# Kernel tuning notes

Hardware: AMD Instinct MI355X
Metric: run time of the kernel (lower is better)

The kernel has to match this reference:

```python
import jax, jax.numpy as jnp
import numpy as np

H, L, D, R = 16, 4096, 64, 128   # heads, seq len, head dim, FAVOR+ feature dim
S_SCALE = 0.125                  # attention inner-product scaling S
CHUNK = 128                      # chunk size for causal linear attention
EPS = 1e-10                      # module's self.epsilon denominator guard


def _get_proj(d, r, seed=0):
    # get_proj(R, D, orthogonal=True, hyperbolic=True): QR-orthogonalized
    # Gaussian block rescaled by chi column norms, then [W, -W].
    rng = np.random.RandomState(seed)
    rh = r // 2
    w = rng.randn(d, rh)
    chis = np.linalg.norm(w, ord=2, axis=0, keepdims=True)
    qm, _ = np.linalg.qr(w, mode='reduced')
    w = qm * chis
    return np.concatenate((w, -w), axis=1).astype(np.float32)  # (D, R)


def setup_inputs() -> dict:
    key = jax.random.key(0)
    kq, kk, kv = jax.random.split(key, 3)
    q = jax.random.normal(kq, (H, L, D), dtype=jnp.float32)
    k = jax.random.normal(kk, (H, L, D), dtype=jnp.float32)
    v = jax.random.normal(kv, (H, L, D), dtype=jnp.float32)
    W = jnp.asarray(_get_proj(D, R))
    return {"T": 64, "k": k, "q": q, "v": v, "W": W}


def _phi(x, W):
    # FAVOR+ feature map: x' = x * S^0.5 / D^0.25;
    # phi(x) = exp(W^T x' - ||x'||^2 / 2) / sqrt(R)
    xs = x * (S_SCALE ** 0.5 / D ** 0.25)            # (H, L, D)
    Wx = jnp.einsum('hld,dr->hlr', xs, W)            # (H, L, R)
    sq = 0.5 * jnp.sum(xs * xs, axis=-1, keepdims=True)
    return jnp.exp(Wx - sq) / (R ** 0.5)             # (H, L, R)


def reference(T, k, q, v, W):
    # Deterministic FAVOR+ estimator of the strictly-causal softmax attention
    # Pred_l = sum_{j<l} v_j exp(S<q_l,k_j>) / sum_{i<l} exp(S<q_l,k_i>)
    # which the tree+sampling machinery approximates (T = sampling budget,
    # irrelevant for the exact kernel estimate). Chunked linear attention.
    del T
    pq = _phi(q, W)                                  # (H, L, R)
    pk = _phi(k, W)                                  # (H, L, R)
    nc = L // CHUNK
    pq_c = pq.reshape(H, nc, CHUNK, R)
    pk_c = pk.reshape(H, nc, CHUNK, R)
    v_c = v.reshape(H, nc, CHUNK, D)
    # per-chunk KV summaries and exclusive prefix over chunks
    skv = jnp.einsum('hncr,hncd->hnrd', pk_c, v_c)   # (H, nc, R, D)
    zk = jnp.sum(pk_c, axis=2)                       # (H, nc, R)
    skv_prev = jnp.cumsum(skv, axis=1) - skv         # exclusive
    zk_prev = jnp.cumsum(zk, axis=1) - zk
    num_inter = jnp.einsum('hncr,hnrd->hncd', pq_c, skv_prev)
    den_inter = jnp.einsum('hncr,hnr->hnc', pq_c, zk_prev)
    # intra-chunk strictly-causal part (j < l)
    A = jnp.einsum('hncr,hnsr->hncs', pq_c, pk_c)    # (H, nc, C, C)
    mask = jnp.tril(jnp.ones((CHUNK, CHUNK), dtype=A.dtype), k=-1)
    A = A * mask
    num_intra = jnp.einsum('hncs,hnsd->hncd', A, v_c)
    den_intra = jnp.sum(A, axis=-1)
    out = (num_inter + num_intra) / (den_inter + den_intra + EPS)[..., None]
    return out.reshape(H, L, D)
```

## Files before the change

### kernel.cpp

```cpp
#include <hip/hip_runtime.h>
#include <hip/hip_cooperative_groups.h>

namespace cg = cooperative_groups;

#define H 16
#define L 4096
#define D 64
#define R 128
#define CHUNK 128
#define NC 32
#define HL (H * L)
#define HN (H * NC)
#define EPS 1e-10f
#define XS_SCALE 0.125f
#define PHI_SCALE 0.08838834764831845f

typedef __attribute__((ext_vector_type(8))) short bf8;
typedef __attribute__((ext_vector_type(4))) short bf4;
typedef __attribute__((ext_vector_type(16))) float facc16;

__device__ __forceinline__ unsigned short f2b(float f) {
    unsigned u = __float_as_uint(f);
    return (unsigned short)((u + 0x7fffu + ((u >> 16) & 1u)) >> 16);
}
__device__ __forceinline__ float b2f(unsigned short s) {
    return __uint_as_float(((unsigned)s) << 16);
}

template<bool DUMP>
__device__ __forceinline__ void phase1(
    const float* __restrict__ q, const float* __restrict__ k,
    const float* __restrict__ v, const float* __restrict__ W,
    unsigned short* bufA, unsigned short* bufB, unsigned short* bufC,
    float* __restrict__ stage, float* __restrict__ zk,
    unsigned short* __restrict__ pqd, unsigned short* __restrict__ pkd,
    unsigned short* __restrict__ vTd, bf8* qf, int hn, int tid)
{
    unsigned short* Wt = bufC;
    unsigned short* xs = bufC + 8192;
    float* sq = (float*)bufB;
    const int lane = tid & 63, wave = tid >> 6, lo = lane & 31, hi = lane >> 5;
    const int l0 = wave * 32;
    const size_t cbase = (size_t)hn * CHUNK * D;

    for (int i = tid; i < 8192; i += 256) {
        int r = i & 127, d = i >> 7;
        Wt[(unsigned)((r * 64 + d) ^ ((r & 7) << 3))] = f2b(W[d * 128 + r]);
    }
    for (int i = tid; i < 2048; i += 256) {
        int row = i >> 4, d0 = (i & 15) * 4;
        float4 vv = *(const float4*)(q + cbase + row * 64 + d0);
        float a0 = vv.x * XS_SCALE, a1 = vv.y * XS_SCALE;
        float a2 = vv.z * XS_SCALE, a3 = vv.w * XS_SCALE;
        float ss = a0 * a0 + a1 * a1 + a2 * a2 + a3 * a3;
        ss += __shfl_xor(ss, 1); ss += __shfl_xor(ss, 2);
        ss += __shfl_xor(ss, 4); ss += __shfl_xor(ss, 8);
        if ((tid & 15) == 0) sq[row] = 0.5f * ss;
        unsigned idx = (unsigned)((row * 64 + d0) ^ ((row & 7) << 3));
        unsigned* p = (unsigned*)&xs[idx];
        p[0] = (unsigned)f2b(a0) | ((unsigned)f2b(a1) << 16);
        p[1] = (unsigned)f2b(a2) | ((unsigned)f2b(a3) << 16);
    }
    __syncthreads();

    {
        facc16 acc[4];
        #pragma unroll
        for (int t = 0; t < 4; ++t)
            #pragma unroll
            for (int e = 0; e < 16; ++e) acc[t][e] = 0.f;
        #pragma unroll
        for (int s = 0; s < 4; ++s) {
            const bf8 a = *(const bf8*)&xs[(unsigned)(((l0 + lo) * 64 + 16 * s + 8 * hi) ^ ((lo & 7) << 3))];
            #pragma unroll
            for (int t = 0; t < 4; ++t) {
                const bf8 b = *(const bf8*)&Wt[(unsigned)(((t * 32 + lo) * 64 + 16 * s + 8 * hi) ^ ((lo & 7) << 3))];
                acc[t] = __builtin_amdgcn_mfma_f32_32x32x16_bf16(a, b, acc[t], 0, 0, 0);
            }
        }
        #pragma unroll
        for (int t = 0; t < 4; ++t)
            #pragma unroll
            for (int reg = 0; reg < 16; ++reg) {
                int row = l0 + (reg & 3) + 8 * (reg >> 2) + 4 * hi;
                int col = t * 32 + lo;
                bufA[(unsigned)((row * 128 + col) ^ ((row & 7) << 3))] =
                    f2b(__expf(acc[t][reg] - sq[row]) * PHI_SCALE);
            }
    }
    __syncthreads();

    #pragma unroll
    for (int s = 0; s < 8; ++s)
        qf[s] = *(const bf8*)&bufA[(unsigned)(((l0 + lo) * 128 + 16 * s + 8 * hi) ^ ((lo & 7) << 3))];
    if constexpr (DUMP) {
        unsigned short* pg = pqd + (size_t)hn * CHUNK * R;
        for (int i = tid; i < 2048; i += 256) {
            int c = i >> 4, rb = (i & 15) * 8;
            *(bf8*)(pg + c * 128 + rb) = *(const bf8*)&bufA[(unsigned)((c * 128 + rb) ^ ((c & 7) << 3))];
        }
    }

    for (int i = tid; i < 2048; i += 256) {
        int row = i >> 4, d0 = (i & 15) * 4;
        float4 vv = *(const float4*)(k + cbase + row * 64 + d0);
        float a0 = vv.x * XS_SCALE, a1 = vv.y * XS_SCALE;
        float a2 = vv.z * XS_SCALE, a3 = vv.w * XS_SCALE;
        float ss = a0 * a0 + a1 * a1 + a2 * a2 + a3 * a3;
        ss += __shfl_xor(ss, 1); ss += __shfl_xor(ss, 2);
        ss += __shfl_xor(ss, 4); ss += __shfl_xor(ss, 8);
        if ((tid & 15) == 0) sq[row] = 0.5f * ss;
        unsigned idx = (unsigned)((row * 64 + d0) ^ ((row & 7) << 3));
        unsigned* p = (unsigned*)&xs[idx];
        p[0] = (unsigned)f2b(a0) | ((unsigned)f2b(a1) << 16);
        p[1] = (unsigned)f2b(a2) | ((unsigned)f2b(a3) << 16);
    }
    __syncthreads();

    facc16 acck[4];
    #pragma unroll
    for (int t = 0; t < 4; ++t)
        #pragma unroll
        for (int e = 0; e < 16; ++e) acck[t][e] = 0.f;
    #pragma unroll
    for (int s = 0; s < 4; ++s) {
        const bf8 a = *(const bf8*)&xs[(unsigned)(((l0 + lo) * 64 + 16 * s + 8 * hi) ^ ((lo & 7) << 3))];
        #pragma unroll
        for (int t = 0; t < 4; ++t) {
            const bf8 b = *(const bf8*)&Wt[(unsigned)(((t * 32 + lo) * 64 + 16 * s + 8 * hi) ^ ((lo & 7) << 3))];
            acck[t] = __builtin_amdgcn_mfma_f32_32x32x16_bf16(a, b, acck[t], 0, 0, 0);
        }
    }
    __syncthreads();

    #pragma unroll
    for (int t = 0; t < 4; ++t) {
        int colr = t * 32 + lo;
        #pragma unroll
        for (int g = 0; g < 4; ++g) {
            int c0 = l0 + 8 * g + 4 * hi;
            bf4 pk4;
            #pragma unroll
            for (int e = 0; e < 4; ++e) {
                unsigned short b = f2b(__expf(acck[t][4 * g + e] - sq[c0 + e]) * PHI_SCALE);
                pk4[e] = (short)b;
                bufA[(unsigned)(((c0 + e) * 128 + colr) ^ (((c0 + e) & 7) << 3))] = b;
            }
            *(bf4*)&bufC[(unsigned)((colr * 128 + c0) ^ ((colr & 7) << 3))] = pk4;
        }
    }
    __syncthreads();

    for (int i = tid; i < 8192; i += 256) {
        int d = i & 63, c = i >> 6;
        bufB[(unsigned)((d * 128 + c) ^ ((d & 7) << 3))] = f2b(v[cbase + c * 64 + d]);
    }
    if (tid < 128) {
        float s = 0.f;
        #pragma unroll
        for (int j = 0; j < 16; ++j) {
            bf8 a8 = *(const bf8*)&bufC[(unsigned)((tid * 128 + 8 * j) ^ ((tid & 7) << 3))];
            #pragma unroll
            for (int e = 0; e < 8; ++e) s += b2f((unsigned short)a8[e]);
        }
        zk[(size_t)hn * 128 + tid] = s;
    }
    if constexpr (DUMP) {
        unsigned short* pg = pkd + (size_t)hn * CHUNK * R;
        for (int i = tid; i < 2048; i += 256) {
            int c = i >> 4, rb = (i & 15) * 8;
            *(bf8*)(pg + c * 128 + rb) = *(const bf8*)&bufA[(unsigned)((c * 128 + rb) ^ ((c & 7) << 3))];
        }
    }
    __syncthreads();

    if constexpr (DUMP) {
        unsigned short* vg2 = vTd + (size_t)hn * D * CHUNK;
        for (int i = tid; i < 1024; i += 256) {
            int d = i >> 4, c0 = (i & 15) * 8;
            *(bf8*)(vg2 + d * 128 + c0) = *(const bf8*)&bufB[(unsigned)((d * 128 + c0) ^ ((d & 7) << 3))];
        }
    }
    {
        facc16 accs[2];
        #pragma unroll
        for (int t = 0; t < 2; ++t)
            #pragma unroll
            for (int e = 0; e < 16; ++e) accs[t][e] = 0.f;
        #pragma unroll
        for (int s = 0; s < 8; ++s) {
            const bf8 b = *(const bf8*)&bufC[(unsigned)(((wave * 32 + lo) * 128 + 16 * s + 8 * hi) ^ ((lo & 7) << 3))];
            #pragma unroll
            for (int db = 0; db < 2; ++db) {
                const bf8 a = *(const bf8*)&bufB[(unsigned)(((db * 32 + lo) * 128 + 16 * s + 8 * hi) ^ ((lo & 7) << 3))];
                accs[db] = __builtin_amdgcn_mfma_f32_32x32x16_bf16(a, b, accs[db], 0, 0, 0);
            }
        }
        float* sg = stage + (size_t)hn * D * R;
        #pragma unroll
        for (int db = 0; db < 2; ++db)
            #pragma unroll
            for (int reg = 0; reg < 16; ++reg) {
                int row = db * 32 + (reg & 3) + 8 * (reg >> 2) + 4 * hi;
                sg[row * 128 + wave * 32 + lo] = accs[db][reg];
            }
    }
}

__device__ __forceinline__ void phase2(const float* __restrict__ stage,
                                       unsigned short* __restrict__ skvTp,
                                       const float* __restrict__ zk,
                                       unsigned short* __restrict__ zkp,
                                       int bid, int tid)
{
    int g = bid * 256 + tid;
    int h2 = g >> 13, dr = g & 8191;
    const float* p = stage + (size_t)h2 * NC * 8192 + dr;
    unsigned short* o = skvTp + (size_t)h2 * NC * 8192 + dr;
    float run = 0.f;
    #pragma unroll
    for (int n = 0; n < NC; ++n) {
        float t = p[(size_t)n * 8192];
        o[(size_t)n * 8192] = f2b(run);
        run += t;
    }
    if (g < 2048) {
        int h3 = g >> 7, r = g & 127;
        const float* pz = zk + (size_t)h3 * NC * 128 + r;
        unsigned short* oz = zkp + (size_t)h3 * NC * 128 + r;
        float runz = 0.f;
        #pragma unroll
        for (int n = 0; n < NC; ++n) {
            float t2 = pz[n * 128];
            oz[n * 128] = f2b(runz);
            runz += t2;
        }
    }
}

__device__ __forceinline__ void phase3(
    unsigned short* bufA, unsigned short* bufB, unsigned short* bufC,
    const unsigned short* __restrict__ skvTp, const unsigned short* __restrict__ zkp,
    const bf8* qf, int hn, int tid, float* __restrict__ out)
{
    const int lane = tid & 63, wave = tid >> 6, lo = lane & 31, hi = lane >> 5;
    const int l0 = wave * 32;
    __syncthreads();

    const unsigned short* svg = skvTp + (size_t)hn * D * R;
    for (int i = tid; i < 1024; i += 256) {
        int d = i >> 4, r0 = (i & 15) * 8;
        *(bf8*)&bufC[(unsigned)((d * 128 + r0) ^ ((d & 7) << 3))] = *(const bf8*)(svg + d * 128 + r0);
    }
    bf8 zf[8], onesf;
    #pragma unroll
    for (int e = 0; e < 8; ++e) onesf[e] = (lo == 0) ? (short)0x3F80 : (short)0;
    #pragma unroll
    for (int s = 0; s < 8; ++s)
        #pragma unroll
        for (int e = 0; e < 8; ++e) zf[s][e] = 0;
    if (lo == 0) {
        #pragma unroll
        for (int s = 0; s < 8; ++s)
            zf[s] = *(const bf8*)(zkp + (size_t)hn * 128 + 16 * s + 8 * hi);
    }

    facc16 acc1[4];
    #pragma unroll
    for (int t = 0; t < 4; ++t)
        #pragma unroll
        for (int e = 0; e < 16; ++e) acc1[t][e] = 0.f;
    #pragma unroll
    for (int s = 0; s < 8; ++s)
        #pragma unroll
        for (int t = 0; t < 4; ++t) {
            const bf8 b = *(const bf8*)&bufA[(unsigned)(((t * 32 + lo) * 128 + 16 * s + 8 * hi) ^ ((lo & 7) << 3))];
            acc1[t] = __builtin_amdgcn_mfma_f32_32x32x16_bf16(qf[s], b, acc1[t], 0, 0, 0);
        }
    __syncthreads();

    #pragma unroll
    for (int t = 0; t < 4; ++t)
        #pragma unroll
        for (int reg = 0; reg < 16; ++reg) {
            int row = l0 + (reg & 3) + 8 * (reg >> 2) + 4 * hi;
            int sc = t * 32 + lo;
            bufA[(unsigned)((row * 128 + sc) ^ ((row & 7) << 3))] = f2b(sc < row ? acc1[t][reg] : 0.f);
        }
    __syncthreads();

    facc16 acc2[3];
    #pragma unroll
    for (int t = 0; t < 3; ++t)
        #pragma unroll
        for (int e = 0; e < 16; ++e) acc2[t][e] = 0.f;
    #pragma unroll
    for (int s = 0; s < 8; ++s) {
        const bf8 a = *(const bf8*)&bufA[(unsigned)(((l0 + lo) * 128 + 16 * s + 8 * hi) ^ ((lo & 7) << 3))];
        #pragma unroll
        for (int t = 0; t < 2; ++t) {
            const bf8 b = *(const bf8*)&bufB[(unsigned)(((t * 32 + lo) * 128 + 16 * s + 8 * hi) ^ ((lo & 7) << 3))];
            acc2[t] = __builtin_amdgcn_mfma_f32_32x32x16_bf16(a, b, acc2[t], 0, 0, 0);
        }
        acc2[2] = __builtin_amdgcn_mfma_f32_32x32x16_bf16(a, onesf, acc2[2], 0, 0, 0);
    }
    #pragma unroll
    for (int s = 0; s < 8; ++s) {
        #pragma unroll
        for (int t = 0; t < 2; ++t) {
            const bf8 b = *(const bf8*)&bufC[(unsigned)(((t * 32 + lo) * 128 + 16 * s + 8 * hi) ^ ((lo & 7) << 3))];
            acc2[t] = __builtin_amdgcn_mfma_f32_32x32x16_bf16(qf[s], b, acc2[t], 0, 0, 0);
        }
        acc2[2] = __builtin_amdgcn_mfma_f32_32x32x16_bf16(qf[s], zf[s], acc2[2], 0, 0, 0);
    }

    float* og = out + (size_t)hn * CHUNK * D;
    #pragma unroll
    for (int reg = 0; reg < 16; ++reg) {
        int row = l0 + (reg & 3) + 8 * (reg >> 2) + 4 * hi;
        float dv = __shfl(acc2[2][reg], lane & 32);
        float inv = 1.0f / (dv + EPS);
        og[row * 64 + lo]      = acc2[0][reg] * inv;
        og[row * 64 + 32 + lo] = acc2[1][reg] * inv;
    }
}

__global__ __launch_bounds__(256, 2) void fused_coop(
    const float* __restrict__ q, const float* __restrict__ k,
    const float* __restrict__ v, const float* __restrict__ W,
    unsigned short* __restrict__ skvTp, unsigned short* __restrict__ zkp,
    float* __restrict__ zk, float* __restrict__ out)
{
    __shared__ __align__(16) unsigned short LDSm[40960];
    unsigned short* bufA = LDSm;
    unsigned short* bufB = LDSm + 16384;
    unsigned short* bufC = LDSm + 24576;
    const int tid = threadIdx.x, hn = blockIdx.x;
    bf8 qf[8];
    phase1<false>(q, k, v, W, bufA, bufB, bufC, out, zk,
                  nullptr, nullptr, nullptr, qf, hn, tid);
    __threadfence();
    cg::this_grid().sync();
    phase2(out, skvTp, zk, zkp, hn, tid);
    __threadfence();
    cg::this_grid().sync();
    __threadfence();
    phase3(bufA, bufB, bufC, skvTp, zkp, qf, hn, tid, out);
}

__global__ __launch_bounds__(256, 2) void kA(
    const float* __restrict__ q, const float* __restrict__ k,
    const float* __restrict__ v, const float* __restrict__ W,
    float* __restrict__ stage, float* __restrict__ zk,
    unsigned short* __restrict__ pqd, unsigned short* __restrict__ pkd,
    unsigned short* __restrict__ vTd)
{
    __shared__ __align__(16) unsigned short LDSm[40960];
    bf8 qf[8];
    phase1<true>(q, k, v, W, LDSm, LDSm + 16384, LDSm + 24576, stage, zk,
                 pqd, pkd, vTd, qf, blockIdx.x, threadIdx.x);
}

__global__ __launch_bounds__(256) void kB(const float* __restrict__ stage,
                                          unsigned short* __restrict__ skvTp,
                                          const float* __restrict__ zk,
                                          unsigned short* __restrict__ zkp)
{
    phase2(stage, skvTp, zk, zkp, blockIdx.x, threadIdx.x);
}

__global__ __launch_bounds__(256, 2) void kC(
    const unsigned short* __restrict__ pq, const unsigned short* __restrict__ pk,
    const unsigned short* __restrict__ vT, const unsigned short* __restrict__ skvTp,
    const unsigned short* __restrict__ zkp, float* __restrict__ out)
{
    __shared__ __align__(16) unsigned short LDSm[32768];
    unsigned short* bufA = LDSm;
    unsigned short* bufB = LDSm + 16384;
    unsigned short* bufC = LDSm + 24576;
    const int tid = threadIdx.x, hn = blockIdx.x;
    const int lane = tid & 63, wave = tid >> 6, lo = lane & 31, hi = lane >> 5;
    const int l0 = wave * 32;

    bf8 qf[8];
    const unsigned short* pqg = pq + (size_t)hn * CHUNK * R;
    #pragma unroll
    for (int s = 0; s < 8; ++s)
        qf[s] = *(const bf8*)(pqg + (l0 + lo) * 128 + 16 * s + 8 * hi);

    const unsigned short* pkg = pk + (size_t)hn * CHUNK * R;
    for (int i = tid; i < 2048; i += 256) {
        int c = i >> 4, rb = (i & 15) * 8;
        *(bf8*)&bufA[(unsigned)((c * 128 + rb) ^ ((c & 7) << 3))] = *(const bf8*)(pkg + c * 128 + rb);
    }
    const unsigned short* vTg = vT + (size_t)hn * D * CHUNK;
    for (int i = tid; i < 1024; i += 256) {
        int d = i >> 4, c0 = (i & 15) * 8;
        *(bf8*)&bufB[(unsigned)((d * 128 + c0) ^ ((d & 7) << 3))] = *(const bf8*)(vTg + d * 128 + c0);
    }
    phase3(bufA, bufB, bufC, skvTp, zkp, qf, hn, tid, out);
}

extern "C" void kernel_launch(void* const* d_in, const int* in_sizes, int n_in,
                              void* d_out, int out_size, void* d_ws, size_t ws_size,
                              hipStream_t stream) {
    const float* k = (const float*)d_in[1];
    const float* q = (const float*)d_in[2];
    const float* v = (const float*)d_in[3];
    const float* W = (const float*)d_in[4];
    float* out = (float*)d_out;

    unsigned short* skvTp = (unsigned short*)d_ws;
    unsigned short* zkp = skvTp + (size_t)HN * D * R;
    float* zk = (float*)(zkp + (size_t)HN * R);
    unsigned short* pq = (unsigned short*)(zk + (size_t)HN * R);
    unsigned short* pk = pq + (size_t)HL * R;
    unsigned short* vT = pk + (size_t)HL * R;

    int nb = 0;
    hipError_t qrc = hipOccupancyMaxActiveBlocksPerMultiprocessor(
        &nb, (const void*)fused_coop, 256, 0);
    bool launched = false;
    if (qrc == hipSuccess && nb >= 2) {
        void* kargs[8] = {(void*)&q, (void*)&k, (void*)&v, (void*)&W,
                          (void*)&skvTp, (void*)&zkp, (void*)&zk, (void*)&out};
        hipError_t rc = hipLaunchCooperativeKernel((const void*)fused_coop,
                                                   dim3(HN), dim3(256), kargs, 0, stream);
        launched = (rc == hipSuccess);
        if (!launched) (void)hipGetLastError();
    }
    if (!launched) {
        kA<<<HN, 256, 0, stream>>>(q, k, v, W, out, zk, pq, pk, vT);
        kB<<<HN, 256, 0, stream>>>(out, skvTp, zk, zkp);
        kC<<<HN, 256, 0, stream>>>(pq, pk, vT, skvTp, zkp, out);
    }
}
```

Baseline: 54.90 us.

## Add 64-row chunk cooperative kernel with prep pass for V and W transposes

Adds a new primary path that uses 64-token chunks, giving 1024 blocks at 4 blocks per CU instead of 512 blocks at 2 per CU. A separate prep kernel pre-transposes V and W to bf16 in global memory, so the fused kernel loads them directly. Row norms are now computed from register fragments with shuffles instead of through LDS. The smaller chunk shortens the intra-chunk work but doubles the sequential prefix length over chunks in phase 2, and adds an extra kernel launch.

```diff
diff --git a/kernel.cpp b/kernel.cpp
--- a/kernel.cpp
+++ b/kernel.cpp
@@ -11,6 +11,9 @@
 #define NC 32
 #define HL (H * L)
 #define HN (H * NC)
+#define C2 64
+#define NC2 64
+#define HN2 (H * NC2)
 #define EPS 1e-10f
 #define XS_SCALE 0.125f
 #define PHI_SCALE 0.08838834764831845f
@@ -25,6 +28,302 @@
 }
 __device__ __forceinline__ float b2f(unsigned short s) {
     return __uint_as_float(((unsigned)s) << 16);
+}
+
+__global__ __launch_bounds__(256) void prep_kernel(const float* __restrict__ v,
+                                                   const float* __restrict__ W,
+                                                   unsigned short* __restrict__ vTg,
+                                                   unsigned short* __restrict__ Wtg) {
+    const int tid = threadIdx.x;
+    if (blockIdx.x < HN2) {
+        __shared__ float vl[64 * 65];
+        const int hn = blockIdx.x;
+        const float* vg = v + (size_t)hn * C2 * D;
+        for (int i = tid; i < 1024; i += 256) {
+            int c = i >> 4, d0 = (i & 15) * 4;
+            float4 t = *(const float4*)(vg + c * 64 + d0);
+            vl[c * 65 + d0] = t.x; vl[c * 65 + d0 + 1] = t.y;
+            vl[c * 65 + d0 + 2] = t.z; vl[c * 65 + d0 + 3] = t.w;
+        }
+        __syncthreads();
+        unsigned short* o = vTg + (size_t)hn * 4096;
+        for (int i = tid; i < 4096; i += 256) {
+            int d = i >> 6;
+            int c = (i & 63) ^ ((d & 7) << 3);
+            o[i] = f2b(vl[c * 65 + d]);
+        }
+    } else {
+        __shared__ float wl[64 * 130];
+        for (int i = tid; i < 8192; i += 256) {
+            int d = i >> 7, r = i & 127;
+            wl[d * 130 + r] = W[i];
+        }
+        __syncthreads();
+        for (int i = tid; i < 8192; i += 256) {
+            int r = i >> 6, d = i & 63;
+            Wtg[i] = f2b(wl[d * 130 + r]);
+        }
+    }
+}
+
+__device__ __forceinline__ void p2_64(unsigned short* __restrict__ skvTp,
+                                      const float* __restrict__ zk,
+                                      unsigned short* __restrict__ zkp,
+                                      int bid, int tid) {
+    int g = bid * 256 + tid;
+    if (g < 131072) {
+        int h = g >> 13, dr = g & 8191;
+        unsigned short* p = skvTp + (size_t)h * NC2 * 8192 + dr;
+        float run = 0.f;
+        #pragma unroll
+        for (int n = 0; n < NC2; ++n) {
+            float t = b2f(p[(size_t)n * 8192]);
+            p[(size_t)n * 8192] = f2b(run);
+            run += t;
+        }
+    } else if (g < 133120) {
+        int g2 = g - 131072;
+        int h = g2 >> 7, r = g2 & 127;
+        const float* pz = zk + (size_t)h * NC2 * 128 + r;
+        unsigned short* oz = zkp + (size_t)h * NC2 * 128 + r;
+        float run = 0.f;
+        #pragma unroll
+        for (int n = 0; n < NC2; ++n) {
+            float t = pz[n * 128];
+            oz[n * 128] = f2b(run);
+            run += t;
+        }
+    }
+}
+
+__global__ __launch_bounds__(256, 4) void fused64(
+    const float* __restrict__ q, const float* __restrict__ k,
+    const unsigned short* __restrict__ vTg, const unsigned short* __restrict__ Wtg,
+    unsigned short* __restrict__ skvTp,
+    float* __restrict__ zk,
+    unsigned short* __restrict__ zkp,
+    float* __restrict__ out)
+{
+    __shared__ __align__(16) unsigned short bufA[8192];
+    __shared__ __align__(16) unsigned short bufB[4096];
+    __shared__ __align__(16) unsigned short bufC[8192];
+    const int tid = threadIdx.x, hn = blockIdx.x;
+    const int lane = tid & 63, wave = tid >> 6, lo = lane & 31, hi = lane >> 5;
+    const int rg = wave & 1;
+    const int ch = wave >> 1;
+    const size_t cbase = (size_t)hn * C2 * D;
+
+    for (int i = tid; i < 1024; i += 256) {
+        int row = i >> 4, d0 = (i & 15) * 4;
+        float4 vv = *(const float4*)(q + cbase + row * 64 + d0);
+        unsigned* p = (unsigned*)&bufB[(unsigned)((row * 64 + d0) ^ ((row & 7) << 3))];
+        p[0] = (unsigned)f2b(vv.x * XS_SCALE) | ((unsigned)f2b(vv.y * XS_SCALE) << 16);
+        p[1] = (unsigned)f2b(vv.z * XS_SCALE) | ((unsigned)f2b(vv.w * XS_SCALE) << 16);
+    }
+    __syncthreads();
+    {
+        bf8 af[4];
+        float ssq = 0.f;
+        #pragma unroll
+        for (int s = 0; s < 4; ++s) {
+            af[s] = *(const bf8*)&bufB[(unsigned)(((rg * 32 + lo) * 64 + 16 * s + 8 * hi) ^ ((lo & 7) << 3))];
+            #pragma unroll
+            for (int e = 0; e < 8; ++e) { float t = b2f((unsigned short)af[s][e]); ssq += t * t; }
+        }
+        ssq += __shfl_xor(ssq, 32); ssq *= 0.5f;
+        float sqrow[16];
+        #pragma unroll
+        for (int reg = 0; reg < 16; ++reg)
+            sqrow[reg] = __shfl(ssq, (reg & 3) + 8 * (reg >> 2) + 4 * hi);
+
+        facc16 acc[2];
+        #pragma unroll
+        for (int t = 0; t < 2; ++t)
+            #pragma unroll
+            for (int e = 0; e < 16; ++e) acc[t][e] = 0.f;
+        #pragma unroll
+        for (int s = 0; s < 4; ++s)
+            #pragma unroll
+            for (int t = 0; t < 2; ++t) {
+                const bf8 b = *(const bf8*)(Wtg + ((2 * ch + t) * 32 + lo) * 64 + 16 * s + 8 * hi);
+                acc[t] = __builtin_amdgcn_mfma_f32_32x32x16_bf16(af[s], b, acc[t], 0, 0, 0);
+            }
+        #pragma unroll
+        for (int t = 0; t < 2; ++t)
+            #pragma unroll
+            for (int reg = 0; reg < 16; ++reg) {
+                int row = rg * 32 + (reg & 3) + 8 * (reg >> 2) + 4 * hi;
+                int col = (2 * ch + t) * 32 + lo;
+                bufC[(unsigned)((row * 128 + col) ^ ((row & 15) << 3))] =
+                    f2b(__expf(acc[t][reg] - sqrow[reg]) * PHI_SCALE);
+            }
+    }
+    __syncthreads();
+
+    bf8 qf[8];
+    #pragma unroll
+    for (int s = 0; s < 8; ++s)
+        qf[s] = *(const bf8*)&bufC[(unsigned)(((rg * 32 + lo) * 128 + 16 * s + 8 * hi) ^ ((lo & 15) << 3))];
+
+    for (int i = tid; i < 1024; i += 256) {
+        int row = i >> 4, d0 = (i & 15) * 4;
+        float4 vv = *(const float4*)(k + cbase + row * 64 + d0);
+        unsigned* p = (unsigned*)&bufB[(unsigned)((row * 64 + d0) ^ ((row & 7) << 3))];
+        p[0] = (unsigned)f2b(vv.x * XS_SCALE) | ((unsigned)f2b(vv.y * XS_SCALE) << 16);
+        p[1] = (unsigned)f2b(vv.z * XS_SCALE) | ((unsigned)f2b(vv.w * XS_SCALE) << 16);
+    }
+    __syncthreads();
+    {
+        bf8 af[4];
+        float ssq = 0.f;
+        #pragma unroll
+        for (int s = 0; s < 4; ++s) {
+            af[s] = *(const bf8*)&bufB[(unsigned)(((rg * 32 + lo) * 64 + 16 * s + 8 * hi) ^ ((lo & 7) << 3))];
+            #pragma unroll
+            for (int e = 0; e < 8; ++e) { float t = b2f((unsigned short)af[s][e]); ssq += t * t; }
+        }
+        ssq += __shfl_xor(ssq, 32); ssq *= 0.5f;
+        float sqrow[16];
+        #pragma unroll
+        for (int reg = 0; reg < 16; ++reg)
+            sqrow[reg] = __shfl(ssq, (reg & 3) + 8 * (reg >> 2) + 4 * hi);
+
+        facc16 acc[2];
+        #pragma unroll
+        for (int t = 0; t < 2; ++t)
+            #pragma unroll
+            for (int e = 0; e < 16; ++e) acc[t][e] = 0.f;
+        #pragma unroll
+        for (int s = 0; s < 4; ++s)
+            #pragma unroll
+            for (int t = 0; t < 2; ++t) {
+                const bf8 b = *(const bf8*)(Wtg + ((2 * ch + t) * 32 + lo) * 64 + 16 * s + 8 * hi);
+                acc[t] = __builtin_amdgcn_mfma_f32_32x32x16_bf16(af[s], b, acc[t], 0, 0, 0);
+            }
+        #pragma unroll
+        for (int t = 0; t < 2; ++t) {
+            int colr = (2 * ch + t) * 32 + lo;
+            #pragma unroll
+            for (int g = 0; g < 4; ++g) {
+                int c0 = rg * 32 + 8 * g + 4 * hi;
+                bf4 pk4;
+                #pragma unroll
+                for (int e = 0; e < 4; ++e) {
+                    unsigned short b = f2b(__expf(acc[t][4 * g + e] - sqrow[4 * g + e]) * PHI_SCALE);
+                    pk4[e] = (short)b;
+                    bufA[(unsigned)(((c0 + e) * 128 + colr) ^ (((c0 + e) & 15) << 3))] = b;
+                }
+                *(bf4*)&bufC[(unsigned)((colr * 64 + c0) ^ ((colr & 7) << 3))] = pk4;
+            }
+        }
+    }
+    __syncthreads();
+
+    for (int i = tid; i < 512; i += 256)
+        *(bf8*)&bufB[i * 8] = *(const bf8*)(vTg + (size_t)hn * 4096 + i * 8);
+    if (tid < 128) {
+        float s = 0.f;
+        #pragma unroll
+        for (int j = 0; j < 8; ++j) {
+            bf8 a8 = *(const bf8*)&bufC[(unsigned)((tid * 64 + 8 * j) ^ ((tid & 7) << 3))];
+            #pragma unroll
+            for (int e = 0; e < 8; ++e) s += b2f((unsigned short)a8[e]);
+        }
+        zk[(size_t)hn * 128 + tid] = s;
+    }
+    __syncthreads();
+
+    {
+        facc16 acs[2];
+        #pragma unroll
+        for (int t = 0; t < 2; ++t)
+            #pragma unroll
+            for (int e = 0; e < 16; ++e) acs[t][e] = 0.f;
+        #pragma unroll
+        for (int s = 0; s < 4; ++s) {
+            const bf8 a = *(const bf8*)&bufB[(unsigned)((((rg) * 32 + lo) * 64 + 16 * s + 8 * hi) ^ ((lo & 7) << 3))];
+            #pragma unroll
+            for (int t = 0; t < 2; ++t) {
+                const bf8 b = *(const bf8*)&bufC[(unsigned)((((2 * ch + t) * 32 + lo) * 64 + 16 * s + 8 * hi) ^ ((lo & 7) << 3))];
+                acs[t] = __builtin_amdgcn_mfma_f32_32x32x16_bf16(a, b, acs[t], 0, 0, 0);
+            }
+        }
+        unsigned short* sg = skvTp + (size_t)hn * 8192;
+        #pragma unroll
+        for (int t = 0; t < 2; ++t)
+            #pragma unroll
+            for (int reg = 0; reg < 16; ++reg) {
+                int d = rg * 32 + (reg & 3) + 8 * (reg >> 2) + 4 * hi;
+                int r = (2 * ch + t) * 32 + lo;
+                sg[d * 128 + r] = f2b(acs[t][reg]);
+            }
+    }
+    __threadfence();
+    cg::this_grid().sync();
+
+    p2_64(skvTp, zk, zkp, hn, tid);
+    __threadfence();
+    cg::this_grid().sync();
+    __threadfence();
+
+    for (int i = tid; i < 512; i += 256) {
+        bf8 t8 = *(const bf8*)(skvTp + (size_t)hn * 8192 + i * 8);
+        int d = i >> 4, r0 = (i & 15) * 8;
+        *(bf8*)&bufC[(unsigned)((d * 128 + r0) ^ ((d & 15) << 3))] = t8;
+    }
+    facc16 ac1;
+    #pragma unroll
+    for (int e = 0; e < 16; ++e) ac1[e] = 0.f;
+    #pragma unroll
+    for (int s = 0; s < 8; ++s) {
+        const bf8 b = *(const bf8*)&bufA[(unsigned)(((ch * 32 + lo) * 128 + 16 * s + 8 * hi) ^ ((lo & 15) << 3))];
+        ac1 = __builtin_amdgcn_mfma_f32_32x32x16_bf16(qf[s], b, ac1, 0, 0, 0);
+    }
+    __syncthreads();
+
+    #pragma unroll
+    for (int reg = 0; reg < 16; ++reg) {
+        int row = rg * 32 + (reg & 3) + 8 * (reg >> 2) + 4 * hi;
+        int sc = ch * 32 + lo;
+        bufA[(unsigned)((row * 64 + sc) ^ ((row & 7) << 3))] = f2b(sc < row ? ac1[reg] : 0.f);
+    }
+    __syncthreads();
+
+    facc16 an, ad;
+    #pragma unroll
+    for (int e = 0; e < 16; ++e) { an[e] = 0.f; ad[e] = 0.f; }
+    bf8 onesf, zf[8];
+    #pragma unroll
+    for (int e = 0; e < 8; ++e) onesf[e] = (lo == 0) ? (short)0x3F80 : (short)0;
+    #pragma unroll
+    for (int s = 0; s < 8; ++s)
+        #pragma unroll
+        for (int e = 0; e < 8; ++e) zf[s][e] = 0;
+    if (lo == 0) {
+        #pragma unroll
+        for (int s = 0; s < 8; ++s)
+            zf[s] = *(const bf8*)(zkp + (size_t)hn * 128 + 16 * s + 8 * hi);
+    }
+    #pragma unroll
+    for (int s = 0; s < 4; ++s) {
+        const bf8 a = *(const bf8*)&bufA[(unsigned)(((rg * 32 + lo) * 64 + 16 * s + 8 * hi) ^ ((lo & 7) << 3))];
+        const bf8 b = *(const bf8*)&bufB[(unsigned)(((ch * 32 + lo) * 64 + 16 * s + 8 * hi) ^ ((lo & 7) << 3))];
+        an = __builtin_amdgcn_mfma_f32_32x32x16_bf16(a, b, an, 0, 0, 0);
+        ad = __builtin_amdgcn_mfma_f32_32x32x16_bf16(a, onesf, ad, 0, 0, 0);
+    }
+    #pragma unroll
+    for (int s = 0; s < 8; ++s) {
+        const bf8 b = *(const bf8*)&bufC[(unsigned)(((ch * 32 + lo) * 128 + 16 * s + 8 * hi) ^ ((lo & 15) << 3))];
+        an = __builtin_amdgcn_mfma_f32_32x32x16_bf16(qf[s], b, an, 0, 0, 0);
+        ad = __builtin_amdgcn_mfma_f32_32x32x16_bf16(qf[s], zf[s], ad, 0, 0, 0);
+    }
+    float* og = out + (size_t)hn * C2 * D;
+    #pragma unroll
+    for (int reg = 0; reg < 16; ++reg) {
+        int row = rg * 32 + (reg & 3) + 8 * (reg >> 2) + 4 * hi;
+        float dv = __shfl(ad[reg], lane & 32);
+        og[row * 64 + ch * 32 + lo] = an[reg] / (dv + EPS);
+    }
 }
 
 template<bool DUMP>
@@ -62,7 +361,6 @@
         p[1] = (unsigned)f2b(a2) | ((unsigned)f2b(a3) << 16);
     }
     __syncthreads();
-
     {
         facc16 acc[4];
         #pragma unroll
@@ -89,7 +387,6 @@
             }
     }
     __syncthreads();
-
     #pragma unroll
     for (int s = 0; s < 8; ++s)
         qf[s] = *(const bf8*)&bufA[(unsigned)(((l0 + lo) * 128 + 16 * s + 8 * hi) ^ ((lo & 7) << 3))];
@@ -100,7 +397,6 @@
             *(bf8*)(pg + c * 128 + rb) = *(const bf8*)&bufA[(unsigned)((c * 128 + rb) ^ ((c & 7) << 3))];
         }
     }
-
     for (int i = tid; i < 2048; i += 256) {
         int row = i >> 4, d0 = (i & 15) * 4;
         float4 vv = *(const float4*)(k + cbase + row * 64 + d0);
@@ -116,7 +412,6 @@
         p[1] = (unsigned)f2b(a2) | ((unsigned)f2b(a3) << 16);
     }
     __syncthreads();
-
     facc16 acck[4];
     #pragma unroll
     for (int t = 0; t < 4; ++t)
@@ -132,7 +427,6 @@
         }
     }
     __syncthreads();
-
     #pragma unroll
     for (int t = 0; t < 4; ++t) {
         int colr = t * 32 + lo;
@@ -150,7 +444,6 @@
         }
     }
     __syncthreads();
-
     for (int i = tid; i < 8192; i += 256) {
         int d = i & 63, c = i >> 6;
         bufB[(unsigned)((d * 128 + c) ^ ((d & 7) << 3))] = f2b(v[cbase + c * 64 + d]);
@@ -173,7 +466,6 @@
         }
     }
     __syncthreads();
-
     if constexpr (DUMP) {
         unsigned short* vg2 = vTd + (size_t)hn * D * CHUNK;
         for (int i = tid; i < 1024; i += 256) {
@@ -246,7 +538,6 @@
     const int lane = tid & 63, wave = tid >> 6, lo = lane & 31, hi = lane >> 5;
     const int l0 = wave * 32;
     __syncthreads();
-
     const unsigned short* svg = skvTp + (size_t)hn * D * R;
     for (int i = tid; i < 1024; i += 256) {
         int d = i >> 4, r0 = (i & 15) * 8;
@@ -264,7 +555,6 @@
         for (int s = 0; s < 8; ++s)
             zf[s] = *(const bf8*)(zkp + (size_t)hn * 128 + 16 * s + 8 * hi);
     }
-
     facc16 acc1[4];
     #pragma unroll
     for (int t = 0; t < 4; ++t)
@@ -278,7 +568,6 @@
             acc1[t] = __builtin_amdgcn_mfma_f32_32x32x16_bf16(qf[s], b, acc1[t], 0, 0, 0);
         }
     __syncthreads();
-
     #pragma unroll
     for (int t = 0; t < 4; ++t)
         #pragma unroll
@@ -288,7 +577,6 @@
             bufA[(unsigned)((row * 128 + sc) ^ ((row & 7) << 3))] = f2b(sc < row ? acc1[t][reg] : 0.f);
         }
     __syncthreads();
-
     facc16 acc2[3];
     #pragma unroll
     for (int t = 0; t < 3; ++t)
@@ -313,7 +601,6 @@
         }
         acc2[2] = __builtin_amdgcn_mfma_f32_32x32x16_bf16(qf[s], zf[s], acc2[2], 0, 0, 0);
     }
-
     float* og = out + (size_t)hn * CHUNK * D;
     #pragma unroll
     for (int reg = 0; reg < 16; ++reg) {
@@ -381,22 +668,20 @@
     const int tid = threadIdx.x, hn = blockIdx.x;
     const int lane = tid & 63, wave = tid >> 6, lo = lane & 31, hi = lane >> 5;
     const int l0 = wave * 32;
-
     bf8 qf[8];
     const unsigned short* pqg = pq + (size_t)hn * CHUNK * R;
     #pragma unroll
     for (int s = 0; s < 8; ++s)
         qf[s] = *(const bf8*)(pqg + (l0 + lo) * 128 + 16 * s + 8 * hi);
-
     const unsigned short* pkg = pk + (size_t)hn * CHUNK * R;
     for (int i = tid; i < 2048; i += 256) {
         int c = i >> 4, rb = (i & 15) * 8;
         *(bf8*)&bufA[(unsigned)((c * 128 + rb) ^ ((c & 7) << 3))] = *(const bf8*)(pkg + c * 128 + rb);
     }
-    const unsigned short* vTg = vT + (size_t)hn * D * CHUNK;
+    const unsigned short* vTg2 = vT + (size_t)hn * D * CHUNK;
     for (int i = tid; i < 1024; i += 256) {
         int d = i >> 4, c0 = (i & 15) * 8;
-        *(bf8*)&bufB[(unsigned)((d * 128 + c0) ^ ((d & 7) << 3))] = *(const bf8*)(vTg + d * 128 + c0);
+        *(bf8*)&bufB[(unsigned)((d * 128 + c0) ^ ((d & 7) << 3))] = *(const bf8*)(vTg2 + d * 128 + c0);
     }
     phase3(bufA, bufB, bufC, skvTp, zkp, qf, hn, tid, out);
 }
@@ -410,6 +695,12 @@
     const float* W = (const float*)d_in[4];
     float* out = (float*)d_out;
 
+    unsigned short* skvTp64 = (unsigned short*)d_ws;
+    float* zk64 = (float*)(skvTp64 + (size_t)HN2 * 8192);
+    unsigned short* zkp64 = (unsigned short*)(zk64 + (size_t)HN2 * 128);
+    unsigned short* vTg = zkp64 + (size_t)HN2 * 128;
+    unsigned short* Wtg = vTg + (size_t)HN2 * 4096;
+
     unsigned short* skvTp = (unsigned short*)d_ws;
     unsigned short* zkp = skvTp + (size_t)HN * D * R;
     float* zk = (float*)(zkp + (size_t)HN * R);
@@ -417,21 +708,30 @@
     unsigned short* pk = pq + (size_t)HL * R;
     unsigned short* vT = pk + (size_t)HL * R;
 
-    int nb = 0;
+    int nb4 = 0;
     hipError_t qrc = hipOccupancyMaxActiveBlocksPerMultiprocessor(
-        &nb, (const void*)fused_coop, 256, 0);
-    bool launched = false;
-    if (qrc == hipSuccess && nb >= 2) {
+        &nb4, (const void*)fused64, 256, 0);
+    if (qrc == hipSuccess && nb4 >= 4) {
+        prep_kernel<<<HN2 + 1, 256, 0, stream>>>(v, W, vTg, Wtg);
+        void* kargs[8] = {(void*)&q, (void*)&k, (void*)&vTg, (void*)&Wtg,
+                          (void*)&skvTp64, (void*)&zk64, (void*)&zkp64, (void*)&out};
+        hipError_t rc = hipLaunchCooperativeKernel((const void*)fused64,
+                                                   dim3(HN2), dim3(256), kargs, 0, stream);
+        if (rc == hipSuccess) return;
+        (void)hipGetLastError();
+    }
+    int nb2 = 0;
+    qrc = hipOccupancyMaxActiveBlocksPerMultiprocessor(
+        &nb2, (const void*)fused_coop, 256, 0);
+    if (qrc == hipSuccess && nb2 >= 2) {
         void* kargs[8] = {(void*)&q, (void*)&k, (void*)&v, (void*)&W,
                           (void*)&skvTp, (void*)&zkp, (void*)&zk, (void*)&out};
         hipError_t rc = hipLaunchCooperativeKernel((const void*)fused_coop,
                                                    dim3(HN), dim3(256), kargs, 0, stream);
-        launched = (rc == hipSuccess);
-        if (!launched) (void)hipGetLastError();
-    }
-    if (!launched) {
-        kA<<<HN, 256, 0, stream>>>(q, k, v, W, out, zk, pq, pk, vT);
-        kB<<<HN, 256, 0, stream>>>(out, skvTp, zk, zkp);
-        kC<<<HN, 256, 0, stream>>>(pq, pk, vT, skvTp, zkp, out);
-    }
-}
+        if (rc == hipSuccess) return;
+        (void)hipGetLastError();
+    }
+    kA<<<HN, 256, 0, stream>>>(q, k, v, W, out, zk, pq, pk, vT);
+    kB<<<HN, 256, 0, stream>>>(out, skvTp, zk, zkp);
+    kC<<<HN, 256, 0, stream>>>(pq, pk, vT, skvTp, zkp, out);
+}
```

New measurement: 55.00 us. About the same (+0.2%).
